# Kernel optimization log

Measured on AMD Instinct MI355X. Metric: run time of the kernel, lower is better.

Reference implementation:

```python
import jax, jax.numpy as jnp
import numpy as np

B, T, D, H, L = 256, 512, 32, 128, 32


def gru_cell(x, h, Wih, Whh, bih, bhh):
    # PyTorch GRU cell: gates ordered (r, z, n)
    gi = x @ Wih.T + bih
    gh = h @ Whh.T + bhh
    ir, iz, inn = jnp.split(gi, 3, axis=-1)
    hr, hz, hn = jnp.split(gh, 3, axis=-1)
    r = jax.nn.sigmoid(ir + hr)
    z = jax.nn.sigmoid(iz + hz)
    n = jnp.tanh(inn + r * hn)
    return (1.0 - z) * n + z * h


def run_dir(x, lengths, Wih, Whh, bih, bhh):
    # Unidirectional GRU over padded batch; masked updates emulate packed sequences:
    # carry at the end equals the hidden state at each sequence's last valid step.
    Bb, Tt, _ = x.shape
    xT = jnp.swapaxes(x, 0, 1)                                   # [T,B,Din]
    mask = (jnp.arange(Tt)[:, None] < lengths[None, :])[:, :, None]  # [T,B,1]
    h0 = jnp.zeros((Bb, Whh.shape[1]), x.dtype)

    def step(h, inp):
        x_t, m = inp
        h_new = gru_cell(x_t, h, Wih, Whh, bih, bhh)
        h = jnp.where(m, h_new, h)
        return h, jnp.where(m, h_new, jnp.zeros_like(h_new))

    h_last, out = jax.lax.scan(step, h0, (xT, mask))
    return jnp.swapaxes(out, 0, 1), h_last


def reverse_seq(x, lengths):
    # Reverse each sequence within its own valid length (positions >= length are junk,
    # callers mask them out).
    Tt = x.shape[1]
    idx = jnp.clip(lengths[:, None] - 1 - jnp.arange(Tt)[None, :], 0)
    return jnp.take_along_axis(x, idx[:, :, None], axis=1)


def vrae_forward(x, eps, enc_Wih0, enc_Whh0, enc_bih0, enc_bhh0,
                 enc_Wih12, enc_Whh12, enc_bih12, enc_bhh12,
                 dec_Wih0, dec_Whh0, dec_bih0, dec_bhh0,
                 dec_Wih1, dec_Whh1, dec_bih1, dec_bhh1,
                 W_mean, b_mean, W_logvar, b_logvar,
                 W_z2h, b_z2h, W_out, b_out, lengths):
    Bb, Tt, _ = x.shape
    valid = (jnp.arange(Tt)[None, :] < lengths[:, None])[:, :, None].astype(x.dtype)

    # --- 3-layer bidirectional encoder (packed-sequence semantics) ---
    seq = x
    for l in range(3):
        if l == 0:
            pf = (enc_Wih0[0], enc_Whh0[0], enc_bih0[0], enc_bhh0[0])
            pb = (enc_Wih0[1], enc_Whh0[1], enc_bih0[1], enc_bhh0[1])
        else:
            pf = (enc_Wih12[l-1, 0], enc_Whh12[l-1, 0], enc_bih12[l-1, 0], enc_bhh12[l-1, 0])
            pb = (enc_Wih12[l-1, 1], enc_Whh12[l-1, 1], enc_bih12[l-1, 1], enc_bhh12[l-1, 1])
        out_f, h_f = run_dir(seq, lengths, *pf)
        out_b_rev, h_b = run_dir(reverse_seq(seq, lengths), lengths, *pb)
        out_b = reverse_seq(out_b_rev, lengths) * valid
        seq = jnp.concatenate([out_f, out_b], axis=-1)

    # hidden[-2] = last-layer forward final, hidden[-1] = last-layer backward final
    hcat = jnp.concatenate([h_f, h_b], axis=-1)                  # [B, 2H]
    mean = hcat @ W_mean.T + b_mean
    logvar = hcat @ W_logvar.T + b_logvar
    z = mean + jnp.exp(0.5 * logvar) * eps

    h_init = jnp.tanh(z @ W_z2h.T + b_z2h)                       # repeated over layers

    def dec_step(carry, _):
        d_in, h1, h2 = carry
        h1n = gru_cell(d_in, h1, dec_Wih0, dec_Whh0, dec_bih0, dec_bhh0)
        h2n = gru_cell(h1n, h2, dec_Wih1, dec_Whh1, dec_bih1, dec_bhh1)
        pred = h2n @ W_out.T + b_out
        return (pred, h1n, h2n), pred

    init = (jnp.zeros((Bb, x.shape[2]), x.dtype), h_init, h_init)
    _, preds = jax.lax.scan(dec_step, init, None, length=Tt)     # [T,B,D]
    reconstruction = jnp.swapaxes(preds, 0, 1)                   # [B,T,D]
    return reconstruction, mean, logvar


def setup_inputs() -> dict:
    key = jax.random.key(0)
    ks = jax.random.split(key, 32)
    s = 0.1
    inp = {}
    inp["x"] = jax.random.normal(ks[0], (B, T, D), jnp.float32)
    lengths = jnp.sort(jax.random.randint(ks[1], (B,), 1, T + 1))[::-1]
    inp["lengths"] = lengths.at[0].set(T).astype(jnp.int32)      # sorted desc, max == T
    inp["eps"] = jax.random.normal(ks[2], (B, L), jnp.float32)
    # encoder layer 0 (input D), stacked over directions [fwd, bwd]
    inp["enc_Wih0"] = jax.random.normal(ks[3], (2, 3 * H, D)) * s
    inp["enc_Whh0"] = jax.random.normal(ks[4], (2, 3 * H, H)) * s
    inp["enc_bih0"] = jax.random.normal(ks[5], (2, 3 * H)) * s
    inp["enc_bhh0"] = jax.random.normal(ks[6], (2, 3 * H)) * s
    # encoder layers 1..2 (input 2H), [layer, dir, ...]
    inp["enc_Wih12"] = jax.random.normal(ks[7], (2, 2, 3 * H, 2 * H)) * s
    inp["enc_Whh12"] = jax.random.normal(ks[8], (2, 2, 3 * H, H)) * s
    inp["enc_bih12"] = jax.random.normal(ks[9], (2, 2, 3 * H)) * s
    inp["enc_bhh12"] = jax.random.normal(ks[10], (2, 2, 3 * H)) * s
    # decoder layer 0 (input D) and layer 1 (input H)
    inp["dec_Wih0"] = jax.random.normal(ks[11], (3 * H, D)) * s
    inp["dec_Whh0"] = jax.random.normal(ks[12], (3 * H, H)) * s
    inp["dec_bih0"] = jax.random.normal(ks[13], (3 * H,)) * s
    inp["dec_bhh0"] = jax.random.normal(ks[14], (3 * H,)) * s
    inp["dec_Wih1"] = jax.random.normal(ks[15], (3 * H, H)) * s
    inp["dec_Whh1"] = jax.random.normal(ks[16], (3 * H, H)) * s
    inp["dec_bih1"] = jax.random.normal(ks[17], (3 * H,)) * s
    inp["dec_bhh1"] = jax.random.normal(ks[18], (3 * H,)) * s
    # linears
    inp["W_mean"] = jax.random.normal(ks[19], (L, 2 * H)) * s
    inp["b_mean"] = jax.random.normal(ks[20], (L,)) * s
    inp["W_logvar"] = jax.random.normal(ks[21], (L, 2 * H)) * s
    inp["b_logvar"] = jax.random.normal(ks[22], (L,)) * s
    inp["W_z2h"] = jax.random.normal(ks[23], (H, L)) * s
    inp["b_z2h"] = jax.random.normal(ks[24], (H,)) * s
    inp["W_out"] = jax.random.normal(ks[25], (D, H)) * s
    inp["b_out"] = jax.random.normal(ks[26], (D,)) * s
    return inp


def reference(x, lengths, eps, enc_Wih0, enc_Whh0, enc_bih0, enc_bhh0,
              enc_Wih12, enc_Whh12, enc_bih12, enc_bhh12,
              dec_Wih0, dec_Whh0, dec_bih0, dec_bhh0,
              dec_Wih1, dec_Whh1, dec_bih1, dec_bhh1,
              W_mean, b_mean, W_logvar, b_logvar,
              W_z2h, b_z2h, W_out, b_out):
    return vrae_forward(x, eps, enc_Wih0, enc_Whh0, enc_bih0, enc_bhh0,
                        enc_Wih12, enc_Whh12, enc_bih12, enc_bhh12,
                        dec_Wih0, dec_Whh0, dec_bih0, dec_bhh0,
                        dec_Wih1, dec_Whh1, dec_bih1, dec_bhh1,
                        W_mean, b_mean, W_logvar, b_logvar,
                        W_z2h, b_z2h, W_out, b_out, lengths)
```

## Files before the change

kernel.cpp:

```cpp
#include <hip/hip_runtime.h>
#include <hip/hip_bf16.h>


typedef __bf16 bf16;
typedef __bf16 bf16x8 __attribute__((ext_vector_type(8)));
typedef float f32x4 __attribute__((ext_vector_type(4)));

#define MFMA(a,b,c) __builtin_amdgcn_mfma_f32_16x16x32_bf16((a),(b),(c),0,0,0)
#define Z4 (f32x4){0.f,0.f,0.f,0.f}

__device__ __forceinline__ float sigm_(float x){ return 1.f/(1.f+__expf(-x)); }
__device__ __forceinline__ float tanh_(float x){
  x = fminf(15.f, fmaxf(-15.f, x));
  float e = __expf(2.f*x);
  return (e-1.f)/(e+1.f);
}
__device__ __forceinline__ float fin_(float v){ return (v - v == 0.0f) ? v : 0.0f; }
__device__ __forceinline__ void pin_(bf16x8 &v){ asm volatile("" : "+v"(v)); }

struct PrepJobs {
  const float* src[9];
  bf16* hi[9];
  bf16* lo[9];
  int n[9];
};

__global__ void prep_w(PrepJobs J){
  const int stride = gridDim.x*blockDim.x;
  const int t0 = blockIdx.x*blockDim.x + threadIdx.x;
  for (int j=0;j<9;++j){
    const float* __restrict__ s = J.src[j];
    bf16* __restrict__ h = J.hi[j];
    bf16* __restrict__ l = J.lo[j];
    const int n = J.n[j];
    for (int i=t0;i<n;i+=stride){
      float v = fin_(s[i]);
      bf16 hh = (bf16)v;
      h[i] = hh;
      l[i] = (bf16)(v - (float)hh);
    }
  }
}

template<int KIN, bool F32IN>
__global__ __launch_bounds__(512,2)
void enc_rec(const void* __restrict__ seqIn_,
             bf16* __restrict__ seqOut,
             const bf16* __restrict__ WihHi_, const bf16* __restrict__ WihLo_,
             const bf16* __restrict__ WhhHi_, const bf16* __restrict__ WhhLo_,
             const float* __restrict__ bih_, const float* __restrict__ bhh_,
             const int* __restrict__ lengths,
             float* __restrict__ hFo, float* __restrict__ hBo)
{
  constexpr int NKS  = KIN/32;
  constexpr int XSTR = F32IN ? 40 : 264;
  constexpr int XPL  = 16*XSTR;
  constexpr int XSLOT= (F32IN?2:1)*XPL;
  const int tid = threadIdx.x;
  const int wave = tid>>6;
  const int lh   = tid&15;
  const int quad = (tid>>4)&3;
  const int dir  = blockIdx.x>>4;
  const int b0   = (blockIdx.x&15)*16;

  const bf16* __restrict__ WihHi = WihHi_ + (size_t)dir*384*KIN;
  const bf16* __restrict__ WihLo = WihLo_ + (size_t)dir*384*KIN;
  const bf16* __restrict__ WhhHi = WhhHi_ + (size_t)dir*384*128;
  const bf16* __restrict__ WhhLo = WhhLo_ + (size_t)dir*384*128;
  const float* __restrict__ bih = bih_ + dir*384;
  const float* __restrict__ bhh = bhh_ + dir*384;

  __shared__ bf16 hHi[16*136], hLo[16*136];
  __shared__ bf16 xb[4*XSLOT];

  const int jc = wave*16 + lh;
  const int cR = jc, cZ = 128+jc, cN = 256+jc;

  bf16x8 wRH[4],wRL[4],wZH[4],wZL[4],wNH[4],wNL[4];
#pragma unroll
  for (int ks=0;ks<4;++ks){
    const int o = ks*32 + quad*8;
    wRH[ks]=*(const bf16x8*)(WhhHi+(size_t)cR*128+o); wRL[ks]=*(const bf16x8*)(WhhLo+(size_t)cR*128+o);
    wZH[ks]=*(const bf16x8*)(WhhHi+(size_t)cZ*128+o); wZL[ks]=*(const bf16x8*)(WhhLo+(size_t)cZ*128+o);
    wNH[ks]=*(const bf16x8*)(WhhHi+(size_t)cN*128+o); wNL[ks]=*(const bf16x8*)(WhhLo+(size_t)cN*128+o);
    pin_(wRH[ks]); pin_(wRL[ks]); pin_(wZH[ks]); pin_(wZL[ks]); pin_(wNH[ks]); pin_(wNL[ks]);
  }
  const float bR  = bih[cR]+bhh[cR];
  const float bZc = bih[cZ]+bhh[cZ];
  const float bNi = bih[cN];
  const float bNh = bhh[cN];

  int lenRow[4];
#pragma unroll
  for (int r=0;r<4;++r) lenRow[r] = lengths[b0 + quad*4 + r];
  const int lenA = lengths[b0+lh];
  const int Tmax = lengths[b0];
  const int TT   = (Tmax+3)&~3;

  const int wrow = (tid>>4)&15;
  const int wcol = (tid&15)*8;
  const int lenW = lengths[b0 + wrow];
  const int srow = tid>>5;
  const int scol = tid&31;
  const int lenS = lengths[b0 + srow];

  for (int i=tid;i<16*136;i+=512){ hHi[i]=(bf16)0.f; hLo[i]=(bf16)0.f; }

  auto stage = [&](int slot, int sabs){
    int tb = dir ? (lenS-1-sabs) : sabs;
    tb = tb<0 ? 0 : (tb>511 ? 511 : tb);
    if constexpr (F32IN){
      float v = ((const float*)seqIn_)[((size_t)(b0+srow)*512+tb)*32 + scol];
      bf16 hh=(bf16)v;
      xb[slot*XSLOT + srow*XSTR + scol] = hh;
      xb[slot*XSLOT + XPL + srow*XSTR + scol] = (bf16)(v-(float)hh);
    } else {
      bf16x8 v = *(const bf16x8*)((const bf16*)seqIn_ + ((size_t)(b0+srow)*512+tb)*256 + scol*8);
      *(bf16x8*)&xb[slot*XSLOT + srow*XSTR + scol*8] = v;
    }
  };
#pragma unroll
  for (int s=0;s<4;++s) stage(s, 1+s);

  f32x4 accR[4], accZ[4], giN[4];
#pragma unroll
  for (int s=0;s<4;++s){ accR[s]=Z4; accZ[s]=Z4; giN[s]=Z4; }

  {
    int tb0 = dir ? (lenA-1) : 0; tb0 = tb0<0?0:tb0;
#pragma unroll
    for (int ks=0;ks<NKS;++ks){
      const int o = ks*32 + quad*8;
      bf16x8 axH, axL;
      if constexpr (F32IN){
        const float* ap = (const float*)seqIn_ + ((size_t)(b0+lh)*512+tb0)*KIN + o;
#pragma unroll
        for (int e=0;e<8;++e){ float v=ap[e]; bf16 hh=(bf16)v; axH[e]=hh; axL[e]=(bf16)(v-(float)hh); }
      } else {
        axH = *(const bf16x8*)((const bf16*)seqIn_ + ((size_t)(b0+lh)*512+tb0)*KIN + o);
      }
      bf16x8 bH, bL;
      bH=*(const bf16x8*)(WihHi+(size_t)cR*KIN+o); bL=*(const bf16x8*)(WihLo+(size_t)cR*KIN+o);
      accR[3]=MFMA(axH,bH,accR[3]); if constexpr(F32IN) accR[3]=MFMA(axL,bH,accR[3]); accR[3]=MFMA(axH,bL,accR[3]);
      bH=*(const bf16x8*)(WihHi+(size_t)cZ*KIN+o); bL=*(const bf16x8*)(WihLo+(size_t)cZ*KIN+o);
      accZ[3]=MFMA(axH,bH,accZ[3]); if constexpr(F32IN) accZ[3]=MFMA(axL,bH,accZ[3]); accZ[3]=MFMA(axH,bL,accZ[3]);
      bH=*(const bf16x8*)(WihHi+(size_t)cN*KIN+o); bL=*(const bf16x8*)(WihLo+(size_t)cN*KIN+o);
      giN[3]=MFMA(axH,bH,giN[3]);  if constexpr(F32IN) giN[3]=MFMA(axL,bH,giN[3]);  giN[3]=MFMA(axH,bL,giN[3]);
    }
  }
  __syncthreads();

  for (int t4=0; t4<TT; t4+=4){
#pragma unroll
    for (int p=0;p<4;++p){
      const int t = t4 + p;
      const int s = (p+3)&3;
      if (seqOut && tid<256 && t>0 && (t-1)<lenW){
        const int tp = t-1;
        const int tb = dir ? (lenW-1-tp) : tp;
        bf16x8 v = *(const bf16x8*)&hHi[wrow*136 + wcol];
        *(bf16x8*)(seqOut + ((size_t)(b0+wrow)*512 + tb)*256 + dir*128 + wcol) = v;
      }
      f32x4 gN = Z4;
#pragma unroll
      for (int ks=0;ks<4;++ks){
        bf16x8 aH = *(const bf16x8*)&hHi[lh*136 + ks*32 + quad*8];
        bf16x8 aL = *(const bf16x8*)&hLo[lh*136 + ks*32 + quad*8];
        accR[s]=MFMA(aH,wRH[ks],accR[s]); accR[s]=MFMA(aL,wRH[ks],accR[s]); accR[s]=MFMA(aH,wRL[ks],accR[s]);
        accZ[s]=MFMA(aH,wZH[ks],accZ[s]); accZ[s]=MFMA(aL,wZH[ks],accZ[s]); accZ[s]=MFMA(aH,wZL[ks],accZ[s]);
        gN     =MFMA(aH,wNH[ks],gN);      gN     =MFMA(aL,wNH[ks],gN);      gN     =MFMA(aH,wNL[ks],gN);
      }
      float hsel[4];
#pragma unroll
      for (int r=0;r<4;++r){
        const int m = quad*4 + r;
        float rr = sigm_(accR[s][r] + bR);
        float zz = sigm_(accZ[s][r] + bZc);
        float nn = tanh_(giN[s][r] + bNi + rr*(gN[r] + bNh));
        float hold = (float)hHi[m*136+jc] + (float)hLo[m*136+jc];
        float hnew = fin_((1.f-zz)*nn + zz*hold);
        hsel[r] = (t < lenRow[r]) ? hnew : hold;
      }
      if (p==0){
#pragma unroll
        for (int s2=0;s2<4;++s2){ accR[s2]=Z4; accZ[s2]=Z4; giN[s2]=Z4; }
#pragma unroll
        for (int ks=0;ks<NKS;++ks){
          const int o = ks*32 + quad*8;
          bf16x8 axH[4], axL[F32IN?4:1];
#pragma unroll
          for (int s2=0;s2<4;++s2){
            axH[s2] = *(const bf16x8*)&xb[s2*XSLOT + lh*XSTR + o];
            if constexpr (F32IN) axL[s2] = *(const bf16x8*)&xb[s2*XSLOT + XPL + lh*XSTR + o];
          }
          bf16x8 bH, bL;
          bH=*(const bf16x8*)(WihHi+(size_t)cR*KIN+o); bL=*(const bf16x8*)(WihLo+(size_t)cR*KIN+o);
#pragma unroll
          for (int s2=0;s2<4;++s2){
            accR[s2]=MFMA(axH[s2],bH,accR[s2]);
            if constexpr(F32IN) accR[s2]=MFMA(axL[s2],bH,accR[s2]);
            accR[s2]=MFMA(axH[s2],bL,accR[s2]);
          }
          bH=*(const bf16x8*)(WihHi+(size_t)cZ*KIN+o); bL=*(const bf16x8*)(WihLo+(size_t)cZ*KIN+o);
#pragma unroll
          for (int s2=0;s2<4;++s2){
            accZ[s2]=MFMA(axH[s2],bH,accZ[s2]);
            if constexpr(F32IN) accZ[s2]=MFMA(axL[s2],bH,accZ[s2]);
            accZ[s2]=MFMA(axH[s2],bL,accZ[s2]);
          }
          bH=*(const bf16x8*)(WihHi+(size_t)cN*KIN+o); bL=*(const bf16x8*)(WihLo+(size_t)cN*KIN+o);
#pragma unroll
          for (int s2=0;s2<4;++s2){
            giN[s2]=MFMA(axH[s2],bH,giN[s2]);
            if constexpr(F32IN) giN[s2]=MFMA(axL[s2],bH,giN[s2]);
            giN[s2]=MFMA(axH[s2],bL,giN[s2]);
          }
        }
      }
      __syncthreads();
#pragma unroll
      for (int r=0;r<4;++r){
        const int m = quad*4 + r;
        bf16 hi = (bf16)hsel[r];
        hHi[m*136+jc] = hi;
        hLo[m*136+jc] = (bf16)(hsel[r]-(float)hi);
      }
      if      (p==1){ stage(0, t4+5); stage(1, t4+6); }
      else if (p==2){ stage(2, t4+7); }
      else if (p==3){ stage(3, t4+8); }
      __syncthreads();
    }
  }
  if (seqOut && tid<256 && (TT-1)<lenW){
    const int tb = dir ? (lenW-1-(TT-1)) : (TT-1);
    bf16x8 v = *(const bf16x8*)&hHi[wrow*136 + wcol];
    *(bf16x8*)(seqOut + ((size_t)(b0+wrow)*512 + tb)*256 + dir*128 + wcol) = v;
  }
  float* hout = dir ? hBo : hFo;
  if (hout && tid<256){
#pragma unroll
    for (int e=0;e<8;++e){
      const int j = wcol+e;
      hout[(size_t)(b0+wrow)*128 + j] = fin_((float)hHi[wrow*136+j] + (float)hLo[wrow*136+j]);
    }
  }
}

__global__ void latent_k(const float* __restrict__ hF, const float* __restrict__ hB,
                         const float* __restrict__ eps,
                         const float* __restrict__ Wm, const float* __restrict__ bm,
                         const float* __restrict__ Wl, const float* __restrict__ bl,
                         const float* __restrict__ Wz, const float* __restrict__ bz,
                         float* __restrict__ out_mean, float* __restrict__ out_logvar,
                         float* __restrict__ hInit)
{
  const int b = blockIdx.x, tid = threadIdx.x;
  __shared__ float hc[256];
  __shared__ float mv[64];
  __shared__ float zz[32];
  for (int k=tid;k<256;k+=64) hc[k] = fin_((k<128)? hF[(size_t)b*128+k] : hB[(size_t)b*128+k-128]);
  __syncthreads();
  {
    const int i = tid & 31;
    const float* W = (tid<32)? Wm : Wl;
    float acc = (tid<32)? bm[i] : bl[i];
    for (int k=0;k<256;++k) acc += hc[k]*W[i*256+k];
    acc = fin_(acc);
    mv[tid] = acc;
    if (tid<32) out_mean[b*32+i] = acc;
    else        out_logvar[b*32+(tid-32)] = acc;
  }
  __syncthreads();
  if (tid<32) zz[tid] = fin_(mv[tid] + __expf(0.5f*mv[32+tid]) * eps[b*32+tid]);
  __syncthreads();
  for (int j=tid;j<128;j+=64){
    float a = bz[j];
    for (int k=0;k<32;++k) a += zz[k]*Wz[j*32+k];
    hInit[(size_t)b*128 + j] = tanh_(fin_(a));
  }
}

__global__ __launch_bounds__(512,2)
void dec_rec(const float* __restrict__ hInit,
             const bf16* __restrict__ W0iH, const bf16* __restrict__ W0iL,
             const bf16* __restrict__ W0hH, const bf16* __restrict__ W0hL,
             const bf16* __restrict__ W1iH, const bf16* __restrict__ W1iL,
             const bf16* __restrict__ W1hH, const bf16* __restrict__ W1hL,
             const bf16* __restrict__ WoH,  const bf16* __restrict__ WoL,
             const float* __restrict__ bih0, const float* __restrict__ bhh0,
             const float* __restrict__ bih1, const float* __restrict__ bhh1,
             const float* __restrict__ bout,
             float* __restrict__ rec)
{
  const int tid = threadIdx.x;
  const int wave = tid>>6;
  const int lh   = tid&15;
  const int quad = (tid>>4)&3;
  const int b0 = blockIdx.x*16;
  const int jc = wave*16 + lh;
  const int cR = jc, cZ = 128+jc, cN = 256+jc;

  __shared__ bf16 h1H[16*136], h1L[16*136], h2H[16*136], h2L[16*136];
  __shared__ bf16 pH[16*40], pL[16*40];
  __shared__ bf16 w1iLds[384*136];

  bf16x8 a0RH[4],a0RL[4],a0ZH[4],a0ZL[4],a0NH[4],a0NL[4];
  bf16x8 a1RH[4],a1RL[4],a1ZH[4],a1ZL[4],a1NH[4],a1NL[4];
#pragma unroll
  for (int ks=0;ks<4;++ks){
    const int o = ks*32 + quad*8;
    a0RH[ks]=*(const bf16x8*)(W0hH+(size_t)cR*128+o); a0RL[ks]=*(const bf16x8*)(W0hL+(size_t)cR*128+o);
    a0ZH[ks]=*(const bf16x8*)(W0hH+(size_t)cZ*128+o); a0ZL[ks]=*(const bf16x8*)(W0hL+(size_t)cZ*128+o);
    a0NH[ks]=*(const bf16x8*)(W0hH+(size_t)cN*128+o); a0NL[ks]=*(const bf16x8*)(W0hL+(size_t)cN*128+o);
    a1RH[ks]=*(const bf16x8*)(W1hH+(size_t)cR*128+o); a1RL[ks]=*(const bf16x8*)(W1hL+(size_t)cR*128+o);
    a1ZH[ks]=*(const bf16x8*)(W1hH+(size_t)cZ*128+o); a1ZL[ks]=*(const bf16x8*)(W1hL+(size_t)cZ*128+o);
    a1NH[ks]=*(const bf16x8*)(W1hH+(size_t)cN*128+o); a1NL[ks]=*(const bf16x8*)(W1hL+(size_t)cN*128+o);
    pin_(a0RH[ks]); pin_(a0RL[ks]); pin_(a0ZH[ks]); pin_(a0ZL[ks]); pin_(a0NH[ks]); pin_(a0NL[ks]);
    pin_(a1RH[ks]); pin_(a1RL[ks]); pin_(a1ZH[ks]); pin_(a1ZL[ks]); pin_(a1NH[ks]); pin_(a1NL[ks]);
  }
  const float b1R = bih0[cR]+bhh0[cR], b1Z = bih0[cZ]+bhh0[cZ], b1Ni = bih0[cN], b1Nh = bhh0[cN];
  const float b2R = bih1[cR]+bhh1[cR], b2Z = bih1[cZ]+bhh1[cZ], b2Ni = bih1[cN], b2Nh = bhh1[cN];
  const float bo = (wave<2) ? bout[wave*16+lh] : 0.f;

  for (int i=tid; i<384*16; i+=512){
    const int rr = i>>4, k8 = (i&15)*8;
    *(bf16x8*)&w1iLds[rr*136 + k8] = *(const bf16x8*)(W1iH + (size_t)rr*128 + k8);
  }
  if (tid < 256){
    const int row = (tid>>4)&15;
    const int c0  = (tid&15)*8;
#pragma unroll
    for (int e=0;e<8;++e){
      const int j = c0+e;
      float v = fin_(hInit[(size_t)(b0+row)*128 + j]);
      bf16 hi=(bf16)v, lo=(bf16)(v-(float)hi);
      h1H[row*136+j]=hi; h1L[row*136+j]=lo;
      h2H[row*136+j]=hi; h2L[row*136+j]=lo;
    }
  }
  for (int i=tid;i<16*40;i+=512){ pH[i]=(bf16)0.f; pL[i]=(bf16)0.f; }
  __syncthreads();

  f32x4 c1R, c1Z, c1Nh, c2R, c2Z, c2Nh;

  auto ghpre = [&](){
    c1R=Z4; c1Z=Z4; c1Nh=Z4; c2R=Z4; c2Z=Z4; c2Nh=Z4;
#pragma unroll
    for (int ks=0;ks<4;++ks){
      const int o = ks*32 + quad*8;
      bf16x8 aH = *(const bf16x8*)&h1H[lh*136 + o];
      bf16x8 aL = *(const bf16x8*)&h1L[lh*136 + o];
      c1R =MFMA(aH,a0RH[ks],c1R);  c1R =MFMA(aL,a0RH[ks],c1R);  c1R =MFMA(aH,a0RL[ks],c1R);
      c1Z =MFMA(aH,a0ZH[ks],c1Z);  c1Z =MFMA(aL,a0ZH[ks],c1Z);  c1Z =MFMA(aH,a0ZL[ks],c1Z);
      c1Nh=MFMA(aH,a0NH[ks],c1Nh); c1Nh=MFMA(aL,a0NH[ks],c1Nh); c1Nh=MFMA(aH,a0NL[ks],c1Nh);
    }
#pragma unroll
    for (int ks=0;ks<4;++ks){
      const int o = ks*32 + quad*8;
      bf16x8 aH = *(const bf16x8*)&h2H[lh*136 + o];
      bf16x8 aL = *(const bf16x8*)&h2L[lh*136 + o];
      c2R =MFMA(aH,a1RH[ks],c2R);  c2R =MFMA(aL,a1RH[ks],c2R);  c2R =MFMA(aH,a1RL[ks],c2R);
      c2Z =MFMA(aH,a1ZH[ks],c2Z);  c2Z =MFMA(aL,a1ZH[ks],c2Z);  c2Z =MFMA(aH,a1ZL[ks],c2Z);
      c2Nh=MFMA(aH,a1NH[ks],c2Nh); c2Nh=MFMA(aL,a1NH[ks],c2Nh); c2Nh=MFMA(aH,a1NL[ks],c2Nh);
    }
  };
  ghpre();

  for (int t=0;t<512;++t){
    {
      f32x4 c1Ni = Z4;
      bf16x8 aP0 = *(const bf16x8*)&pH[lh*40 + quad*8];
      bf16x8 aP1 = *(const bf16x8*)&pL[lh*40 + quad*8];
      const int o = quad*8;
      bf16x8 bH,bL;
      bH=*(const bf16x8*)(W0iH+(size_t)cR*32+o); bL=*(const bf16x8*)(W0iL+(size_t)cR*32+o);
      c1R=MFMA(aP0,bH,c1R); c1R=MFMA(aP1,bH,c1R); c1R=MFMA(aP0,bL,c1R);
      bH=*(const bf16x8*)(W0iH+(size_t)cZ*32+o); bL=*(const bf16x8*)(W0iL+(size_t)cZ*32+o);
      c1Z=MFMA(aP0,bH,c1Z); c1Z=MFMA(aP1,bH,c1Z); c1Z=MFMA(aP0,bL,c1Z);
      bH=*(const bf16x8*)(W0iH+(size_t)cN*32+o); bL=*(const bf16x8*)(W0iL+(size_t)cN*32+o);
      c1Ni=MFMA(aP0,bH,c1Ni); c1Ni=MFMA(aP1,bH,c1Ni); c1Ni=MFMA(aP0,bL,c1Ni);
#pragma unroll
      for (int r=0;r<4;++r){
        const int m = quad*4+r;
        float rr = sigm_(c1R[r] + b1R);
        float z  = sigm_(c1Z[r] + b1Z);
        float nn = tanh_(c1Ni[r] + b1Ni + rr*(c1Nh[r] + b1Nh));
        float hold = (float)h1H[m*136+jc] + (float)h1L[m*136+jc];
        float hnew = fin_((1.f-z)*nn + z*hold);
        bf16 hi=(bf16)hnew;
        h1H[m*136+jc]=hi; h1L[m*136+jc]=(bf16)(hnew-(float)hi);
      }
    }
    __syncthreads();
    {
      f32x4 c2Ni = Z4;
#pragma unroll
      for (int ks=0;ks<4;++ks){
        const int o = ks*32 + quad*8;
        bf16x8 aH = *(const bf16x8*)&h1H[lh*136 + o];
        bf16x8 aL = *(const bf16x8*)&h1L[lh*136 + o];
        bf16x8 bH,bL;
        bH=*(const bf16x8*)&w1iLds[cR*136+o]; bL=*(const bf16x8*)(W1iL+(size_t)cR*128+o);
        c2R=MFMA(aH,bH,c2R); c2R=MFMA(aL,bH,c2R); c2R=MFMA(aH,bL,c2R);
        bH=*(const bf16x8*)&w1iLds[cZ*136+o]; bL=*(const bf16x8*)(W1iL+(size_t)cZ*128+o);
        c2Z=MFMA(aH,bH,c2Z); c2Z=MFMA(aL,bH,c2Z); c2Z=MFMA(aH,bL,c2Z);
        bH=*(const bf16x8*)&w1iLds[cN*136+o]; bL=*(const bf16x8*)(W1iL+(size_t)cN*128+o);
        c2Ni=MFMA(aH,bH,c2Ni); c2Ni=MFMA(aL,bH,c2Ni); c2Ni=MFMA(aH,bL,c2Ni);
      }
#pragma unroll
      for (int r=0;r<4;++r){
        const int m = quad*4+r;
        float rr = sigm_(c2R[r] + b2R);
        float z  = sigm_(c2Z[r] + b2Z);
        float nn = tanh_(c2Ni[r] + b2Ni + rr*(c2Nh[r] + b2Nh));
        float hold = (float)h2H[m*136+jc] + (float)h2L[m*136+jc];
        float hnew = fin_((1.f-z)*nn + z*hold);
        bf16 hi=(bf16)hnew;
        h2H[m*136+jc]=hi; h2L[m*136+jc]=(bf16)(hnew-(float)hi);
      }
    }
    __syncthreads();
    if (wave<2){
      f32x4 po=Z4;
#pragma unroll
      for (int ks=0;ks<4;++ks){
        const int o = ks*32 + quad*8;
        bf16x8 oH = *(const bf16x8*)&h2H[lh*136 + o];
        bf16x8 oL = *(const bf16x8*)&h2L[lh*136 + o];
        bf16x8 bH = *(const bf16x8*)(WoH + (size_t)(wave*16+lh)*128 + o);
        bf16x8 bL = *(const bf16x8*)(WoL + (size_t)(wave*16+lh)*128 + o);
        po=MFMA(oH,bH,po); po=MFMA(oL,bH,po); po=MFMA(oH,bL,po);
      }
#pragma unroll
      for (int r=0;r<4;++r){
        const int m = quad*4+r;
        float pv = fin_(po[r]+bo);
        rec[((size_t)(b0+m)*512 + t)*32 + wave*16+lh] = pv;
        bf16 hi=(bf16)pv;
        pH[m*40 + wave*16+lh]=hi; pL[m*40 + wave*16+lh]=(bf16)(pv-(float)hi);
      }
    }
    if (t+1 < 512) ghpre();
    __syncthreads();
  }
}

extern "C" void kernel_launch(void* const* d_in, const int* in_sizes, int n_in,
                              void* d_out, int out_size, void* d_ws, size_t ws_size,
                              hipStream_t stream)
{
  const float* x       = (const float*)d_in[0];
  const int*   lengths = (const int*)d_in[1];
  const float* eps     = (const float*)d_in[2];
  const float* eWih0   = (const float*)d_in[3];
  const float* eWhh0   = (const float*)d_in[4];
  const float* ebih0   = (const float*)d_in[5];
  const float* ebhh0   = (const float*)d_in[6];
  const float* eWih12  = (const float*)d_in[7];
  const float* eWhh12  = (const float*)d_in[8];
  const float* ebih12  = (const float*)d_in[9];
  const float* ebhh12  = (const float*)d_in[10];
  const float* dWih0   = (const float*)d_in[11];
  const float* dWhh0   = (const float*)d_in[12];
  const float* dbih0   = (const float*)d_in[13];
  const float* dbhh0   = (const float*)d_in[14];
  const float* dWih1   = (const float*)d_in[15];
  const float* dWhh1   = (const float*)d_in[16];
  const float* dbih1   = (const float*)d_in[17];
  const float* dbhh1   = (const float*)d_in[18];
  const float* Wm      = (const float*)d_in[19];
  const float* bm      = (const float*)d_in[20];
  const float* Wl      = (const float*)d_in[21];
  const float* bl      = (const float*)d_in[22];
  const float* Wz      = (const float*)d_in[23];
  const float* bz      = (const float*)d_in[24];
  const float* Wo      = (const float*)d_in[25];
  const float* bo      = (const float*)d_in[26];

  char* ws = (char*)d_ws;
  bf16* P     = (bf16*)ws;
  bf16* seqA  = (bf16*)(ws + (size_t)(4<<20));
  bf16* seqB  = (bf16*)(ws + (size_t)(68<<20));
  float* hF    = (float*)seqA;
  float* hB    = hF + 256*128;
  float* hInit = hB + 256*128;

  const size_t O_eWih0  = 0;
  const size_t O_eWhh0  = 49152;
  const size_t O_eWih12 = 245760;
  const size_t O_eWhh12 = 1032192;
  const size_t O_dWih0  = 1425408;
  const size_t O_dWhh0  = 1449984;
  const size_t O_dWih1  = 1548288;
  const size_t O_dWhh1  = 1646592;
  const size_t O_Wout   = 1744896;

  float* out   = (float*)d_out;
  float* rec   = out;
  float* omean = out + (size_t)4194304;
  float* ologv = omean + 8192;

  size_t zoff = (size_t)(4<<20);
  size_t zbytes = (size_t)(128<<20);
  if (zoff + zbytes > ws_size) zbytes = (ws_size > zoff)? ws_size - zoff : 0;
  hipMemsetAsync(ws + zoff, 0, zbytes, stream);

  PrepJobs J;
  const float* srcs[9] = {eWih0, eWhh0, eWih12, eWhh12, dWih0, dWhh0, dWih1, dWhh1, Wo};
  const size_t offs[9] = {O_eWih0,O_eWhh0,O_eWih12,O_eWhh12,O_dWih0,O_dWhh0,O_dWih1,O_dWhh1,O_Wout};
  const int    ns[9]   = {24576, 98304, 393216, 196608, 12288, 49152, 49152, 49152, 4096};
  for (int j=0;j<9;++j){ J.src[j]=srcs[j]; J.hi[j]=P+offs[j]; J.lo[j]=P+offs[j]+ns[j]; J.n[j]=ns[j]; }
  prep_w<<<256, 256, 0, stream>>>(J);

  dim3 blk(512);

  enc_rec<32,true><<<32, blk, 0, stream>>>(x, seqA,
      P+O_eWih0, P+O_eWih0+24576, P+O_eWhh0, P+O_eWhh0+98304,
      ebih0, ebhh0, lengths, nullptr, nullptr);
  enc_rec<256,false><<<32, blk, 0, stream>>>(seqA, seqB,
      P+O_eWih12, P+O_eWih12+393216, P+O_eWhh12, P+O_eWhh12+196608,
      ebih12, ebhh12, lengths, nullptr, nullptr);
  enc_rec<256,false><<<32, blk, 0, stream>>>(seqB, nullptr,
      P+O_eWih12+196608, P+O_eWih12+393216+196608,
      P+O_eWhh12+98304,  P+O_eWhh12+196608+98304,
      ebih12+768, ebhh12+768, lengths, hF, hB);
  latent_k<<<256, 64, 0, stream>>>(hF, hB, eps, Wm, bm, Wl, bl, Wz, bz,
                                   omean, ologv, hInit);
  dec_rec<<<16, blk, 0, stream>>>(hInit,
      P+O_dWih0, P+O_dWih0+12288, P+O_dWhh0, P+O_dWhh0+49152,
      P+O_dWih1, P+O_dWih1+49152, P+O_dWhh1, P+O_dWhh1+49152,
      P+O_Wout,  P+O_Wout+4096,
      dbih0, dbhh0, dbih1, dbhh1, bo, rec);
}
```

Before: 9.803 ms.

## Split encoder block into recurrence and input-projection warp groups with gate ring

Each encoder block grows to 768 threads. Eight waves run only the recurrent h·Whh MFMAs and the gate math. Four extra waves stage inputs, compute the input projection for the next four timesteps into a five-slot fp32 ring buffer in shared memory, and write the output sequence. This takes the bursty x·Wih work off the serial critical path of the recurrence waves. The cost is a large shared-memory ring (about 120KB), occupancy pinned to three waves per EU, and gate pre-activations read from LDS instead of registers.

```diff
diff --git a/kernel.cpp b/kernel.cpp
--- a/kernel.cpp
+++ b/kernel.cpp
@@ -43,7 +43,7 @@
 }
 
 template<int KIN, bool F32IN>
-__global__ __launch_bounds__(512,2)
+__global__ __launch_bounds__(768) __attribute__((amdgpu_waves_per_eu(3,3)))
 void enc_rec(const void* __restrict__ seqIn_,
              bf16* __restrict__ seqOut,
              const bf16* __restrict__ WihHi_, const bf16* __restrict__ WihLo_,
@@ -56,12 +56,13 @@
   constexpr int XSTR = F32IN ? 40 : 264;
   constexpr int XPL  = 16*XSTR;
   constexpr int XSLOT= (F32IN?2:1)*XPL;
-  const int tid = threadIdx.x;
+  const int tid  = threadIdx.x;
   const int wave = tid>>6;
   const int lh   = tid&15;
   const int quad = (tid>>4)&3;
   const int dir  = blockIdx.x>>4;
   const int b0   = (blockIdx.x&15)*16;
+  const bool ghR = (tid < 512);
 
   const bf16* __restrict__ WihHi = WihHi_ + (size_t)dir*384*KIN;
   const bf16* __restrict__ WihLo = WihLo_ + (size_t)dir*384*KIN;
@@ -70,178 +71,201 @@
   const float* __restrict__ bih = bih_ + dir*384;
   const float* __restrict__ bhh = bhh_ + dir*384;
 
+  __shared__ float ring[5*16*384];
   __shared__ bf16 hHi[16*136], hLo[16*136];
-  __shared__ bf16 xb[4*XSLOT];
+  __shared__ bf16 xb[3*XSLOT];
+
+  const int Tmax = lengths[b0];
+  const int TT   = (Tmax+3)&~3;
+  const int lenA = lengths[b0+lh];
+
+  for (int i=tid;i<16*136;i+=768){ hHi[i]=(bf16)0.f; hLo[i]=(bf16)0.f; }
 
   const int jc = wave*16 + lh;
   const int cR = jc, cZ = 128+jc, cN = 256+jc;
-
   bf16x8 wRH[4],wRL[4],wZH[4],wZL[4],wNH[4],wNL[4];
-#pragma unroll
-  for (int ks=0;ks<4;++ks){
-    const int o = ks*32 + quad*8;
-    wRH[ks]=*(const bf16x8*)(WhhHi+(size_t)cR*128+o); wRL[ks]=*(const bf16x8*)(WhhLo+(size_t)cR*128+o);
-    wZH[ks]=*(const bf16x8*)(WhhHi+(size_t)cZ*128+o); wZL[ks]=*(const bf16x8*)(WhhLo+(size_t)cZ*128+o);
-    wNH[ks]=*(const bf16x8*)(WhhHi+(size_t)cN*128+o); wNL[ks]=*(const bf16x8*)(WhhLo+(size_t)cN*128+o);
-    pin_(wRH[ks]); pin_(wRL[ks]); pin_(wZH[ks]); pin_(wZL[ks]); pin_(wNH[ks]); pin_(wNL[ks]);
-  }
-  const float bR  = bih[cR]+bhh[cR];
-  const float bZc = bih[cZ]+bhh[cZ];
-  const float bNi = bih[cN];
-  const float bNh = bhh[cN];
-
-  int lenRow[4];
-#pragma unroll
-  for (int r=0;r<4;++r) lenRow[r] = lengths[b0 + quad*4 + r];
-  const int lenA = lengths[b0+lh];
-  const int Tmax = lengths[b0];
-  const int TT   = (Tmax+3)&~3;
-
-  const int wrow = (tid>>4)&15;
-  const int wcol = (tid&15)*8;
-  const int lenW = lengths[b0 + wrow];
-  const int srow = tid>>5;
-  const int scol = tid&31;
-  const int lenS = lengths[b0 + srow];
-
-  for (int i=tid;i<16*136;i+=512){ hHi[i]=(bf16)0.f; hLo[i]=(bf16)0.f; }
-
-  auto stage = [&](int slot, int sabs){
-    int tb = dir ? (lenS-1-sabs) : sabs;
+  float bR=0.f,bZ=0.f,bNi=0.f,bNh=0.f;
+  int lenRow[4]={0,0,0,0};
+  if (ghR){
+#pragma unroll
+    for (int ks=0;ks<4;++ks){
+      const int o = ks*32 + quad*8;
+      wRH[ks]=*(const bf16x8*)(WhhHi+(size_t)cR*128+o); wRL[ks]=*(const bf16x8*)(WhhLo+(size_t)cR*128+o);
+      wZH[ks]=*(const bf16x8*)(WhhHi+(size_t)cZ*128+o); wZL[ks]=*(const bf16x8*)(WhhLo+(size_t)cZ*128+o);
+      wNH[ks]=*(const bf16x8*)(WhhHi+(size_t)cN*128+o); wNL[ks]=*(const bf16x8*)(WhhLo+(size_t)cN*128+o);
+      pin_(wRH[ks]); pin_(wRL[ks]); pin_(wZH[ks]); pin_(wZL[ks]); pin_(wNH[ks]); pin_(wNL[ks]);
+    }
+    bR  = bih[cR]+bhh[cR];
+    bZ  = bih[cZ]+bhh[cZ];
+    bNi = bih[cN];
+    bNh = bhh[cN];
+#pragma unroll
+    for (int r=0;r<4;++r) lenRow[r] = lengths[b0 + quad*4 + r];
+  }
+
+  const int sIdx = tid - 512;
+  const int jc0  = (wave-8)*32 + lh;
+  const int jc1  = jc0 + 16;
+  const int wrow = (sIdx>>4)&15, wcol=(sIdx&15)*8;
+  int lenW = 0;
+  if (!ghR) lenW = lengths[b0 + wrow];
+
+  auto stageB = [&](int linear, int baseStep){
+    const int slot = linear>>9;
+    const int idx  = linear&511;
+    const int srow = idx>>5;
+    const int sabs = baseStep + slot;
+    const int ls   = lengths[b0+srow];
+    int tb = dir ? ls-1-sabs : sabs;
     tb = tb<0 ? 0 : (tb>511 ? 511 : tb);
     if constexpr (F32IN){
+      const int scol = idx&31;
       float v = ((const float*)seqIn_)[((size_t)(b0+srow)*512+tb)*32 + scol];
       bf16 hh=(bf16)v;
       xb[slot*XSLOT + srow*XSTR + scol] = hh;
       xb[slot*XSLOT + XPL + srow*XSTR + scol] = (bf16)(v-(float)hh);
     } else {
-      bf16x8 v = *(const bf16x8*)((const bf16*)seqIn_ + ((size_t)(b0+srow)*512+tb)*256 + scol*8);
-      *(bf16x8*)&xb[slot*XSLOT + srow*XSTR + scol*8] = v;
+      const int sblk = idx&31;
+      bf16x8 v = *(const bf16x8*)((const bf16*)seqIn_ + ((size_t)(b0+srow)*512+tb)*256 + sblk*8);
+      *(bf16x8*)&xb[slot*XSLOT + srow*XSTR + sblk*8] = v;
     }
   };
-#pragma unroll
-  for (int s=0;s<4;++s) stage(s, 1+s);
-
-  f32x4 accR[4], accZ[4], giN[4];
-#pragma unroll
-  for (int s=0;s<4;++s){ accR[s]=Z4; accZ[s]=Z4; giN[s]=Z4; }
-
-  {
-    int tb0 = dir ? (lenA-1) : 0; tb0 = tb0<0?0:tb0;
-#pragma unroll
-    for (int ks=0;ks<NKS;++ks){
-      const int o = ks*32 + quad*8;
-      bf16x8 axH, axL;
-      if constexpr (F32IN){
-        const float* ap = (const float*)seqIn_ + ((size_t)(b0+lh)*512+tb0)*KIN + o;
-#pragma unroll
-        for (int e=0;e<8;++e){ float v=ap[e]; bf16 hh=(bf16)v; axH[e]=hh; axL[e]=(bf16)(v-(float)hh); }
+
+  auto sweep = [&](int base){
+    const int s3 = base+3;
+    int tb3 = dir ? lenA-1-s3 : s3;
+    tb3 = tb3<0 ? 0 : (tb3>511 ? 511 : tb3);
+    const int r0=(base)%5, r1=(base+1)%5, r2=(base+2)%5, r3=(base+3)%5;
+#pragma unroll
+    for (int tg=0; tg<6; ++tg){
+      const int col = ((tg<3)? jc0 : jc1) + (tg%3)*128;
+      const bf16* bHp = WihHi + (size_t)col*KIN;
+      const bf16* bLp = WihLo + (size_t)col*KIN;
+      f32x4 a0=Z4,a1=Z4,a2=Z4,a3=Z4;
+#pragma unroll
+      for (int ks=0;ks<NKS;++ks){
+        const int o = ks*32 + quad*8;
+        bf16x8 bH = *(const bf16x8*)(bHp + o);
+        bf16x8 bL = *(const bf16x8*)(bLp + o);
+        if constexpr (F32IN){
+          bf16x8 xh, xl;
+          xh = *(const bf16x8*)&xb[0*XSLOT + lh*XSTR + o];
+          xl = *(const bf16x8*)&xb[0*XSLOT + XPL + lh*XSTR + o];
+          a0=MFMA(xh,bH,a0); a0=MFMA(xl,bH,a0); a0=MFMA(xh,bL,a0);
+          xh = *(const bf16x8*)&xb[1*XSLOT + lh*XSTR + o];
+          xl = *(const bf16x8*)&xb[1*XSLOT + XPL + lh*XSTR + o];
+          a1=MFMA(xh,bH,a1); a1=MFMA(xl,bH,a1); a1=MFMA(xh,bL,a1);
+          xh = *(const bf16x8*)&xb[2*XSLOT + lh*XSTR + o];
+          xl = *(const bf16x8*)&xb[2*XSLOT + XPL + lh*XSTR + o];
+          a2=MFMA(xh,bH,a2); a2=MFMA(xl,bH,a2); a2=MFMA(xh,bL,a2);
+          const float* xp = (const float*)seqIn_ + ((size_t)(b0+lh)*512+tb3)*KIN + o;
+          bf16x8 x3h, x3l;
+#pragma unroll
+          for (int e=0;e<8;++e){ float v=xp[e]; bf16 hh=(bf16)v; x3h[e]=hh; x3l[e]=(bf16)(v-(float)hh); }
+          a3=MFMA(x3h,bH,a3); a3=MFMA(x3l,bH,a3); a3=MFMA(x3h,bL,a3);
+        } else {
+          bf16x8 x0 = *(const bf16x8*)&xb[0*XSLOT + lh*XSTR + o];
+          a0=MFMA(x0,bH,a0); a0=MFMA(x0,bL,a0);
+          bf16x8 x1 = *(const bf16x8*)&xb[1*XSLOT + lh*XSTR + o];
+          a1=MFMA(x1,bH,a1); a1=MFMA(x1,bL,a1);
+          bf16x8 x2 = *(const bf16x8*)&xb[2*XSLOT + lh*XSTR + o];
+          a2=MFMA(x2,bH,a2); a2=MFMA(x2,bL,a2);
+          bf16x8 x3 = *(const bf16x8*)((const bf16*)seqIn_ + ((size_t)(b0+lh)*512+tb3)*KIN + o);
+          a3=MFMA(x3,bH,a3); a3=MFMA(x3,bL,a3);
+        }
+      }
+#pragma unroll
+      for (int r=0;r<4;++r){
+        const int m = quad*4+r;
+        ring[r0*6144 + m*384 + col] = a0[r];
+        ring[r1*6144 + m*384 + col] = a1[r];
+        ring[r2*6144 + m*384 + col] = a2[r];
+        ring[r3*6144 + m*384 + col] = a3[r];
+      }
+    }
+  };
+
+  if (!ghR){
+#pragma unroll
+    for (int u=0;u<6;++u) stageB(u*256 + sIdx, 0);
+  }
+  __syncthreads();
+  if (!ghR) sweep(0);
+  __syncthreads();
+
+  for (int t4=0; t4<TT; t4+=4){
+#pragma unroll
+    for (int p=0;p<4;++p){
+      const int t = t4+p;
+      float hsel[4];
+      if (ghR){
+        f32x4 gR=Z4, gZ=Z4, gN=Z4;
+#pragma unroll
+        for (int ks=0;ks<4;++ks){
+          bf16x8 aH = *(const bf16x8*)&hHi[lh*136 + ks*32 + quad*8];
+          bf16x8 aL = *(const bf16x8*)&hLo[lh*136 + ks*32 + quad*8];
+          gR=MFMA(aH,wRH[ks],gR); gR=MFMA(aL,wRH[ks],gR); gR=MFMA(aH,wRL[ks],gR);
+          gZ=MFMA(aH,wZH[ks],gZ); gZ=MFMA(aL,wZH[ks],gZ); gZ=MFMA(aH,wZL[ks],gZ);
+          gN=MFMA(aH,wNH[ks],gN); gN=MFMA(aL,wNH[ks],gN); gN=MFMA(aH,wNL[ks],gN);
+        }
+        const int rs = t%5;
+#pragma unroll
+        for (int r=0;r<4;++r){
+          const int m = quad*4+r;
+          const float giR = ring[rs*6144 + m*384 + cR];
+          const float giZ = ring[rs*6144 + m*384 + cZ];
+          const float giN = ring[rs*6144 + m*384 + cN];
+          float rr = sigm_(gR[r] + giR + bR);
+          float zz = sigm_(gZ[r] + giZ + bZ);
+          float nn = tanh_(giN + bNi + rr*(gN[r] + bNh));
+          float hold = (float)hHi[m*136+jc] + (float)hLo[m*136+jc];
+          float hnew = fin_((1.f-zz)*nn + zz*hold);
+          hsel[r] = (t < lenRow[r]) ? hnew : hold;
+        }
       } else {
-        axH = *(const bf16x8*)((const bf16*)seqIn_ + ((size_t)(b0+lh)*512+tb0)*KIN + o);
-      }
-      bf16x8 bH, bL;
-      bH=*(const bf16x8*)(WihHi+(size_t)cR*KIN+o); bL=*(const bf16x8*)(WihLo+(size_t)cR*KIN+o);
-      accR[3]=MFMA(axH,bH,accR[3]); if constexpr(F32IN) accR[3]=MFMA(axL,bH,accR[3]); accR[3]=MFMA(axH,bL,accR[3]);
-      bH=*(const bf16x8*)(WihHi+(size_t)cZ*KIN+o); bL=*(const bf16x8*)(WihLo+(size_t)cZ*KIN+o);
-      accZ[3]=MFMA(axH,bH,accZ[3]); if constexpr(F32IN) accZ[3]=MFMA(axL,bH,accZ[3]); accZ[3]=MFMA(axH,bL,accZ[3]);
-      bH=*(const bf16x8*)(WihHi+(size_t)cN*KIN+o); bL=*(const bf16x8*)(WihLo+(size_t)cN*KIN+o);
-      giN[3]=MFMA(axH,bH,giN[3]);  if constexpr(F32IN) giN[3]=MFMA(axL,bH,giN[3]);  giN[3]=MFMA(axH,bL,giN[3]);
-    }
-  }
-  __syncthreads();
-
-  for (int t4=0; t4<TT; t4+=4){
-#pragma unroll
-    for (int p=0;p<4;++p){
-      const int t = t4 + p;
-      const int s = (p+3)&3;
-      if (seqOut && tid<256 && t>0 && (t-1)<lenW){
-        const int tp = t-1;
-        const int tb = dir ? (lenW-1-tp) : tp;
-        bf16x8 v = *(const bf16x8*)&hHi[wrow*136 + wcol];
-        *(bf16x8*)(seqOut + ((size_t)(b0+wrow)*512 + tb)*256 + dir*128 + wcol) = v;
-      }
-      f32x4 gN = Z4;
-#pragma unroll
-      for (int ks=0;ks<4;++ks){
-        bf16x8 aH = *(const bf16x8*)&hHi[lh*136 + ks*32 + quad*8];
-        bf16x8 aL = *(const bf16x8*)&hLo[lh*136 + ks*32 + quad*8];
-        accR[s]=MFMA(aH,wRH[ks],accR[s]); accR[s]=MFMA(aL,wRH[ks],accR[s]); accR[s]=MFMA(aH,wRL[ks],accR[s]);
-        accZ[s]=MFMA(aH,wZH[ks],accZ[s]); accZ[s]=MFMA(aL,wZH[ks],accZ[s]); accZ[s]=MFMA(aH,wZL[ks],accZ[s]);
-        gN     =MFMA(aH,wNH[ks],gN);      gN     =MFMA(aL,wNH[ks],gN);      gN     =MFMA(aH,wNL[ks],gN);
-      }
-      float hsel[4];
-#pragma unroll
-      for (int r=0;r<4;++r){
-        const int m = quad*4 + r;
-        float rr = sigm_(accR[s][r] + bR);
-        float zz = sigm_(accZ[s][r] + bZc);
-        float nn = tanh_(giN[s][r] + bNi + rr*(gN[r] + bNh));
-        float hold = (float)hHi[m*136+jc] + (float)hLo[m*136+jc];
-        float hnew = fin_((1.f-zz)*nn + zz*hold);
-        hsel[r] = (t < lenRow[r]) ? hnew : hold;
-      }
-      if (p==0){
-#pragma unroll
-        for (int s2=0;s2<4;++s2){ accR[s2]=Z4; accZ[s2]=Z4; giN[s2]=Z4; }
-#pragma unroll
-        for (int ks=0;ks<NKS;++ks){
-          const int o = ks*32 + quad*8;
-          bf16x8 axH[4], axL[F32IN?4:1];
-#pragma unroll
-          for (int s2=0;s2<4;++s2){
-            axH[s2] = *(const bf16x8*)&xb[s2*XSLOT + lh*XSTR + o];
-            if constexpr (F32IN) axL[s2] = *(const bf16x8*)&xb[s2*XSLOT + XPL + lh*XSTR + o];
-          }
-          bf16x8 bH, bL;
-          bH=*(const bf16x8*)(WihHi+(size_t)cR*KIN+o); bL=*(const bf16x8*)(WihLo+(size_t)cR*KIN+o);
-#pragma unroll
-          for (int s2=0;s2<4;++s2){
-            accR[s2]=MFMA(axH[s2],bH,accR[s2]);
-            if constexpr(F32IN) accR[s2]=MFMA(axL[s2],bH,accR[s2]);
-            accR[s2]=MFMA(axH[s2],bL,accR[s2]);
-          }
-          bH=*(const bf16x8*)(WihHi+(size_t)cZ*KIN+o); bL=*(const bf16x8*)(WihLo+(size_t)cZ*KIN+o);
-#pragma unroll
-          for (int s2=0;s2<4;++s2){
-            accZ[s2]=MFMA(axH[s2],bH,accZ[s2]);
-            if constexpr(F32IN) accZ[s2]=MFMA(axL[s2],bH,accZ[s2]);
-            accZ[s2]=MFMA(axH[s2],bL,accZ[s2]);
-          }
-          bH=*(const bf16x8*)(WihHi+(size_t)cN*KIN+o); bL=*(const bf16x8*)(WihLo+(size_t)cN*KIN+o);
-#pragma unroll
-          for (int s2=0;s2<4;++s2){
-            giN[s2]=MFMA(axH[s2],bH,giN[s2]);
-            if constexpr(F32IN) giN[s2]=MFMA(axL[s2],bH,giN[s2]);
-            giN[s2]=MFMA(axH[s2],bL,giN[s2]);
-          }
+        if (seqOut && t>0 && (t-1)<lenW){
+          const int tp = t-1;
+          const int tb = dir ? (lenW-1-tp) : tp;
+          bf16x8 v = *(const bf16x8*)&hHi[wrow*136 + wcol];
+          *(bf16x8*)(seqOut + ((size_t)(b0+wrow)*512 + tb)*256 + dir*128 + wcol) = v;
         }
+        if (p==0){
+#pragma unroll
+          for (int u=0;u<4;++u) stageB(u*256 + sIdx, t4+4);
+        } else if (p==1){
+#pragma unroll
+          for (int u=0;u<2;++u) stageB(1024 + u*256 + sIdx, t4+4);
+        } else if (p==3){
+          sweep(t4+4);
+        }
       }
       __syncthreads();
-#pragma unroll
-      for (int r=0;r<4;++r){
-        const int m = quad*4 + r;
-        bf16 hi = (bf16)hsel[r];
-        hHi[m*136+jc] = hi;
-        hLo[m*136+jc] = (bf16)(hsel[r]-(float)hi);
-      }
-      if      (p==1){ stage(0, t4+5); stage(1, t4+6); }
-      else if (p==2){ stage(2, t4+7); }
-      else if (p==3){ stage(3, t4+8); }
+      if (ghR){
+#pragma unroll
+        for (int r=0;r<4;++r){
+          const int m = quad*4+r;
+          bf16 hi = (bf16)hsel[r];
+          hHi[m*136+jc] = hi;
+          hLo[m*136+jc] = (bf16)(hsel[r]-(float)hi);
+        }
+      }
       __syncthreads();
     }
   }
-  if (seqOut && tid<256 && (TT-1)<lenW){
-    const int tb = dir ? (lenW-1-(TT-1)) : (TT-1);
-    bf16x8 v = *(const bf16x8*)&hHi[wrow*136 + wcol];
-    *(bf16x8*)(seqOut + ((size_t)(b0+wrow)*512 + tb)*256 + dir*128 + wcol) = v;
-  }
-  float* hout = dir ? hBo : hFo;
-  if (hout && tid<256){
-#pragma unroll
-    for (int e=0;e<8;++e){
-      const int j = wcol+e;
-      hout[(size_t)(b0+wrow)*128 + j] = fin_((float)hHi[wrow*136+j] + (float)hLo[wrow*136+j]);
+
+  if (!ghR){
+    if (seqOut && (TT-1)<lenW){
+      const int tb = dir ? (lenW-1-(TT-1)) : (TT-1);
+      bf16x8 v = *(const bf16x8*)&hHi[wrow*136 + wcol];
+      *(bf16x8*)(seqOut + ((size_t)(b0+wrow)*512 + tb)*256 + dir*128 + wcol) = v;
+    }
+    float* hout = dir ? hBo : hFo;
+    if (hout){
+#pragma unroll
+      for (int e=0;e<8;++e){
+        const int j = wcol+e;
+        hout[(size_t)(b0+wrow)*128 + j] = fin_((float)hHi[wrow*136+j] + (float)hLo[wrow*136+j]);
+      }
     }
   }
 }
@@ -280,7 +304,7 @@
   }
 }
 
-__global__ __launch_bounds__(512,2)
+__global__ __launch_bounds__(512) __attribute__((amdgpu_waves_per_eu(2,2)))
 void dec_rec(const float* __restrict__ hInit,
              const bf16* __restrict__ W0iH, const bf16* __restrict__ W0iL,
              const bf16* __restrict__ W0hH, const bf16* __restrict__ W0hL,
@@ -512,21 +536,21 @@
   for (int j=0;j<9;++j){ J.src[j]=srcs[j]; J.hi[j]=P+offs[j]; J.lo[j]=P+offs[j]+ns[j]; J.n[j]=ns[j]; }
   prep_w<<<256, 256, 0, stream>>>(J);
 
-  dim3 blk(512);
-
-  enc_rec<32,true><<<32, blk, 0, stream>>>(x, seqA,
+  dim3 blkE(768), blkD(512);
+
+  enc_rec<32,true><<<32, blkE, 0, stream>>>(x, seqA,
       P+O_eWih0, P+O_eWih0+24576, P+O_eWhh0, P+O_eWhh0+98304,
       ebih0, ebhh0, lengths, nullptr, nullptr);
-  enc_rec<256,false><<<32, blk, 0, stream>>>(seqA, seqB,
+  enc_rec<256,false><<<32, blkE, 0, stream>>>(seqA, seqB,
       P+O_eWih12, P+O_eWih12+393216, P+O_eWhh12, P+O_eWhh12+196608,
       ebih12, ebhh12, lengths, nullptr, nullptr);
-  enc_rec<256,false><<<32, blk, 0, stream>>>(seqB, nullptr,
+  enc_rec<256,false><<<32, blkE, 0, stream>>>(seqB, nullptr,
       P+O_eWih12+196608, P+O_eWih12+393216+196608,
       P+O_eWhh12+98304,  P+O_eWhh12+196608+98304,
       ebih12+768, ebhh12+768, lengths, hF, hB);
   latent_k<<<256, 64, 0, stream>>>(hF, hB, eps, Wm, bm, Wl, bl, Wz, bz,
                                    omean, ologv, hInit);
-  dec_rec<<<16, blk, 0, stream>>>(hInit,
+  dec_rec<<<16, blkD, 0, stream>>>(hInit,
       P+O_dWih0, P+O_dWih0+12288, P+O_dWhh0, P+O_dWhh0+49152,
       P+O_dWih1, P+O_dWih1+49152, P+O_dWhh1, P+O_dWhh1+49152,
       P+O_Wout,  P+O_Wout+4096,
```

Measured after the change: 21.56 ms. 120% more time.
